# Optimization experiments

Hardware: AMD Instinct MI355X
Metric: run time of the kernel (lower is better)

Reference implementation:

```python
import jax, jax.numpy as jnp
import numpy as np

HEAD_NUM = 16
EMB_DIM = 1024
PROJ_DIM = 1024
CONTEXT_LEN = 2048
HEAD_DIM = PROJ_DIM // HEAD_NUM


def setup_inputs() -> dict:
    key = jax.random.key(0)
    k_x, k_q, k_k, k_v, k_o = jax.random.split(key, 5)
    scale = 0.02
    X_emb = jax.random.normal(k_x, (2, CONTEXT_LEN, EMB_DIM), dtype=jnp.float32)
    W_q = jax.random.normal(k_q, (EMB_DIM, PROJ_DIM), dtype=jnp.float32) * scale
    W_k = jax.random.normal(k_k, (EMB_DIM, PROJ_DIM), dtype=jnp.float32) * scale
    W_v = jax.random.normal(k_v, (EMB_DIM, PROJ_DIM), dtype=jnp.float32) * scale
    W_out = jax.random.normal(k_o, (PROJ_DIM, PROJ_DIM), dtype=jnp.float32) * scale
    return {"X_emb": X_emb, "W_q": W_q, "W_k": W_k, "W_v": W_v, "W_out": W_out}


def reference(X_emb, W_q, W_k, W_v, W_out):
    B, S, _ = X_emb.shape
    H, D = HEAD_NUM, HEAD_DIM
    # QKV projections (no bias), split into heads: [B, H, S, D]
    q = (X_emb @ W_q).reshape(B, S, H, D).transpose(0, 2, 1, 3)
    k = (X_emb @ W_k).reshape(B, S, H, D).transpose(0, 2, 1, 3)
    v = (X_emb @ W_v).reshape(B, S, H, D).transpose(0, 2, 1, 3)
    # Raw scores [B, H, S, S]; causal mask applied BEFORE scaling (as in source;
    # -inf is invariant under the subsequent division so math matches).
    scores = jnp.einsum("bhqd,bhkd->bhqk", q, k)
    causal = jnp.triu(jnp.ones((S, S), dtype=bool), k=1)  # True above diagonal
    scores = jnp.where(causal, -jnp.inf, scores)
    scores = scores / jnp.asarray(np.sqrt(D), dtype=scores.dtype)
    att_w = jax.nn.softmax(scores, axis=-1)
    # dropout_rate = 0.0 -> identity
    ctx = jnp.einsum("bhqk,bhkd->bhqd", att_w, v)
    ctx = ctx.transpose(0, 2, 1, 3).reshape(B, S, H * D)
    return ctx @ W_out
```

## Files before the change

### kernel.cpp

```cpp
#include <hip/hip_runtime.h>
#include <stdint.h>

#define SEQ   2048
#define EMB   1024
#define PROJ  1024
#define HEADS 16
#define HD    64
#define BATCH 2
#define MROWS (BATCH * SEQ)
#define QKVN  3072

typedef __attribute__((ext_vector_type(8))) __bf16 bf16x8;
typedef __attribute__((ext_vector_type(4))) __bf16 bf16x4;
typedef __attribute__((ext_vector_type(4))) float  f32x4;

static __device__ __forceinline__ __bf16 f2b(float f) {
  union { float f; uint32_t u; } a; a.f = f;
  uint32_t r = a.u + 0x7FFFu + ((a.u >> 16) & 1u);
  union { uint16_t u; __bf16 b; } o; o.u = (uint16_t)(r >> 16);
  return o.b;
}

#define GLOAD_LDS16(gsrc, ldst)                                                \
  __builtin_amdgcn_global_load_lds(                                            \
      (const __attribute__((address_space(1))) void*)(gsrc),                   \
      (__attribute__((address_space(3))) void*)(ldst), 16, 0, 0)

__global__ void cast_f32_bf16(const float* __restrict__ in,
                              __bf16* __restrict__ out, int n) {
  int i = (blockIdx.x * blockDim.x + threadIdx.x) * 4;
  if (i + 3 < n) {
    float4 v = *reinterpret_cast<const float4*>(in + i);
    bf16x4 o;
    o[0] = f2b(v.x); o[1] = f2b(v.y); o[2] = f2b(v.z); o[3] = f2b(v.w);
    *reinterpret_cast<bf16x4*>(out + i) = o;
  }
}

__global__ void transpose_cast(const float* __restrict__ W0, const float* __restrict__ W1,
                               const float* __restrict__ W2, const float* __restrict__ W3,
                               __bf16* __restrict__ Tqkv, __bf16* __restrict__ To) {
  const float* W; __bf16* T;
  switch (blockIdx.z) {
    case 0: W = W0; T = Tqkv;                       break;
    case 1: W = W1; T = Tqkv + (size_t)1024 * 1024; break;
    case 2: W = W2; T = Tqkv + (size_t)2048 * 1024; break;
    default: W = W3; T = To;                        break;
  }
  __shared__ float tile[32][33];
  int k0 = blockIdx.x * 32, n0 = blockIdx.y * 32;
  int tx = threadIdx.x & 31, ty = threadIdx.x >> 5;
#pragma unroll
  for (int r = ty; r < 32; r += 8)
    tile[r][tx] = W[(size_t)(k0 + r) * 1024 + n0 + tx];
  __syncthreads();
#pragma unroll
  for (int r = ty; r < 32; r += 8)
    T[(size_t)(n0 + r) * 1024 + k0 + tx] = f2b(tile[tx][r]);
}

template <int BM, bool OUT_BF16, bool SCALE_Q, bool VSPLIT>
__global__ __launch_bounds__(256) void gemm_bt(const __bf16* __restrict__ A,
                                               const __bf16* __restrict__ Bt,
                                               void* __restrict__ Cout,
                                               __bf16* __restrict__ vt,
                                               int M, int N, int K) {
  constexpr int MI = BM / 32;
  __shared__ __align__(16) __bf16 As[BM * 32];
  __shared__ __align__(16) __bf16 Bs[128 * 32];
  const int t = threadIdx.x;
  const int lane = t & 63, w = t >> 6;
  const int g = lane >> 4, l15 = lane & 15;
  const int m0 = blockIdx.x * BM, n0 = blockIdx.y * 128;
  const int wr = w >> 1, wc = w & 1;

  f32x4 acc[MI][4];
#pragma unroll
  for (int i = 0; i < MI; i++)
#pragma unroll
    for (int j = 0; j < 4; j++) acc[i][j] = {0.f, 0.f, 0.f, 0.f};

  for (int k0 = 0; k0 < K; k0 += 32) {
    __syncthreads();
#pragma unroll
    for (int c = t; c < BM * 4; c += 256)
      GLOAD_LDS16(A + (size_t)(m0 + (c >> 2)) * K + k0 + (c & 3) * 8, As + c * 8);
#pragma unroll
    for (int c = t; c < 512; c += 256)
      GLOAD_LDS16(Bt + (size_t)(n0 + (c >> 2)) * K + k0 + (c & 3) * 8, Bs + c * 8);
    __syncthreads();

    bf16x8 af[MI], bfr[4];
#pragma unroll
    for (int mi = 0; mi < MI; mi++)
      af[mi] = *reinterpret_cast<const bf16x8*>(As + (wr * (BM / 2) + mi * 16 + l15) * 32 + g * 8);
#pragma unroll
    for (int ni = 0; ni < 4; ni++)
      bfr[ni] = *reinterpret_cast<const bf16x8*>(Bs + (wc * 64 + ni * 16 + l15) * 32 + g * 8);
#pragma unroll
    for (int mi = 0; mi < MI; mi++)
#pragma unroll
      for (int ni = 0; ni < 4; ni++)
        acc[mi][ni] = __builtin_amdgcn_mfma_f32_16x16x32_bf16(af[mi], bfr[ni], acc[mi][ni], 0, 0, 0);
  }

#pragma unroll
  for (int mi = 0; mi < MI; mi++)
#pragma unroll
    for (int ni = 0; ni < 4; ni++) {
      int row = m0 + wr * (BM / 2) + mi * 16 + g * 4;
      int col = n0 + wc * 64 + ni * 16 + l15;
      if (VSPLIT && col >= 2048) {
        int hd = col - 2048;
        int bb = row >> 11, ss = row & 2047;
        bf16x4 v4;
#pragma unroll
        for (int r = 0; r < 4; r++) v4[r] = f2b(acc[mi][ni][r]);
        *reinterpret_cast<bf16x4*>(vt + ((size_t)((bb * 16 + (hd >> 6)) * 64 + (hd & 63))) * 2048 + ss) = v4;
      } else {
#pragma unroll
        for (int r = 0; r < 4; r++) {
          float v = acc[mi][ni][r];
          if (SCALE_Q && col < 1024) v *= 0.125f;
          if (OUT_BF16)
            ((__bf16*)Cout)[(size_t)(row + r) * N + col] = f2b(v);
          else
            ((float*)Cout)[(size_t)(row + r) * N + col] = v;
        }
      }
    }
}

__global__ __launch_bounds__(256, 2) void attn_fwd(const __bf16* __restrict__ QKV,
                                                   const __bf16* __restrict__ Vt,
                                                   __bf16* __restrict__ ctx) {
  const int id = blockIdx.x;
  const int bh = (id & 7) * 4 + ((id >> 3) & 3);
  const int mi = 31 - (id >> 5);
  const int b = bh >> 4, h = bh & 15;
  const int tid = threadIdx.x, lane = tid & 63, w = tid >> 6;
  const int g = lane >> 4, l15 = lane & 15;

  __shared__ __align__(16) __bf16 Ks[2][64 * 64];
  __shared__ __align__(16) __bf16 Vs[2][64 * 64];
  __shared__ __align__(16) __bf16 P_lds[4][16][72];

  const __bf16* Qg  = QKV + (size_t)b * SEQ * QKVN + h * 64;
  const __bf16* Kg  = Qg + 1024;
  const __bf16* VtH = Vt + (size_t)bh * 64 * 2048;
  __bf16* Cg = ctx + (size_t)b * SEQ * 1024 + h * 64;

  const int r0 = tid >> 3, j0 = tid & 7;
  const int r1 = r0 + 32;
  const int ls0 = r0 * 64 + ((j0 ^ (r0 & 7)) * 8);
  const int ls1 = r1 * 64 + ((j0 ^ (r1 & 7)) * 8);
  const size_t gk0 = (size_t)r0 * QKVN + j0 * 8;
  const size_t gk1 = (size_t)r1 * QKVN + j0 * 8;
  const size_t gv0 = (size_t)r0 * 2048 + j0 * 8;
  const size_t gv1 = (size_t)r1 * 2048 + j0 * 8;
  const int xw = l15 & 7;

  const int qw = mi * 64 + 16 * w;
  const int Tm = mi + 1;

  bf16x8 qf[2];
#pragma unroll
  for (int ks = 0; ks < 2; ks++)
    qf[ks] = *reinterpret_cast<const bf16x8*>(
        Qg + (size_t)(qw + l15) * QKVN + ks * 32 + g * 8);

  f32x4 acco[4];
  float mrun = -1e30f, lrun = 0.f;
#pragma unroll
  for (int nd = 0; nd < 4; nd++) acco[nd] = {0.f, 0.f, 0.f, 0.f};

  {
    bf16x8 ka = *reinterpret_cast<const bf16x8*>(Kg + gk0);
    bf16x8 kb = *reinterpret_cast<const bf16x8*>(Kg + gk1);
    bf16x8 va = *reinterpret_cast<const bf16x8*>(VtH + gv0);
    bf16x8 vc = *reinterpret_cast<const bf16x8*>(VtH + gv1);
    *reinterpret_cast<bf16x8*>(Ks[0] + ls0) = ka;
    *reinterpret_cast<bf16x8*>(Ks[0] + ls1) = kb;
    *reinterpret_cast<bf16x8*>(Vs[0] + ls0) = va;
    *reinterpret_cast<bf16x8*>(Vs[0] + ls1) = vc;
  }
  __syncthreads();

  for (int it = 0; it < Tm; ++it) {
    const int cur = it & 1, nxt = cur ^ 1;
    const bool hn = (it + 1 < Tm);
    bf16x8 ka, kb, va, vc;
    if (hn) {
      const size_t kvn = (size_t)(it + 1) * 64;
      ka = *reinterpret_cast<const bf16x8*>(Kg + kvn * QKVN + gk0);
      kb = *reinterpret_cast<const bf16x8*>(Kg + kvn * QKVN + gk1);
      va = *reinterpret_cast<const bf16x8*>(VtH + kvn + gv0);
      vc = *reinterpret_cast<const bf16x8*>(VtH + kvn + gv1);
    }

    {
      const int kv0 = it * 64;
      const bool diag = (it == Tm - 1);
      const __bf16* Kc = Ks[cur];
      const __bf16* Vc = Vs[cur];

      bf16x8 kf[4][2], vb[4][2];
#pragma unroll
      for (int nb = 0; nb < 4; nb++) {
        const int row = (nb * 16 + l15) * 64;
#pragma unroll
        for (int ks = 0; ks < 2; ks++) {
          const int co = ((ks * 4 + g) ^ xw) * 8;
          kf[nb][ks] = *reinterpret_cast<const bf16x8*>(Kc + row + co);
          vb[nb][ks] = *reinterpret_cast<const bf16x8*>(Vc + row + co);
        }
      }

      f32x4 accS[4];
#pragma unroll
      for (int nb = 0; nb < 4; nb++) accS[nb] = {0.f, 0.f, 0.f, 0.f};
      __builtin_amdgcn_s_setprio(1);
#pragma unroll
      for (int nb = 0; nb < 4; nb++) {
        accS[nb] = __builtin_amdgcn_mfma_f32_16x16x32_bf16(kf[nb][0], qf[0], accS[nb], 0, 0, 0);
        accS[nb] = __builtin_amdgcn_mfma_f32_16x16x32_bf16(kf[nb][1], qf[1], accS[nb], 0, 0, 0);
      }
      __builtin_amdgcn_s_setprio(0);

      if (diag) {
        const int qi = qw + l15;
#pragma unroll
        for (int nb = 0; nb < 4; nb++)
#pragma unroll
          for (int r = 0; r < 4; r++) {
            int kvi = kv0 + nb * 16 + g * 4 + r;
            if (kvi > qi) accS[nb][r] = -1e30f;
          }
      }

      {
        float pmax = -1e30f;
#pragma unroll
        for (int nb = 0; nb < 4; nb++)
#pragma unroll
          for (int r = 0; r < 4; r++) pmax = fmaxf(pmax, accS[nb][r]);
        pmax = fmaxf(pmax, __shfl_xor(pmax, 16));
        pmax = fmaxf(pmax, __shfl_xor(pmax, 32));
        if (!__all(pmax <= mrun + 8.0f)) {
          float mnew = fmaxf(mrun, pmax);
          float corr = __expf(mrun - mnew);
          mrun = mnew;
          lrun *= corr;
#pragma unroll
          for (int r = 0; r < 4; r++) {
            float cr = __shfl(corr, (g << 4) + (g << 2) + r);
#pragma unroll
            for (int nd = 0; nd < 4; nd++) acco[nd][r] *= cr;
          }
        }
        float lsum = 0.f;
#pragma unroll
        for (int nb = 0; nb < 4; nb++) {
          bf16x4 pk;
#pragma unroll
          for (int r = 0; r < 4; r++) {
            float pv = __expf(accS[nb][r] - mrun);
            lsum += pv;
            pk[r] = (__bf16)pv;
          }
          *reinterpret_cast<bf16x4*>(&P_lds[w][l15][nb * 16 + g * 4]) = pk;
        }
        lsum += __shfl_xor(lsum, 16);
        lsum += __shfl_xor(lsum, 32);
        lrun += lsum;
      }

      {
        bf16x8 pa0 = *reinterpret_cast<const bf16x8*>(&P_lds[w][l15][g * 8]);
        bf16x8 pa1 = *reinterpret_cast<const bf16x8*>(&P_lds[w][l15][32 + g * 8]);
        __builtin_amdgcn_s_setprio(1);
#pragma unroll
        for (int nd = 0; nd < 4; nd++) {
          acco[nd] = __builtin_amdgcn_mfma_f32_16x16x32_bf16(pa0, vb[nd][0], acco[nd], 0, 0, 0);
          acco[nd] = __builtin_amdgcn_mfma_f32_16x16x32_bf16(pa1, vb[nd][1], acco[nd], 0, 0, 0);
        }
        __builtin_amdgcn_s_setprio(0);
      }
    }

    if (hn) {
      *reinterpret_cast<bf16x8*>(Ks[nxt] + ls0) = ka;
      *reinterpret_cast<bf16x8*>(Ks[nxt] + ls1) = kb;
      *reinterpret_cast<bf16x8*>(Vs[nxt] + ls0) = va;
      *reinterpret_cast<bf16x8*>(Vs[nxt] + ls1) = vc;
    }
    __syncthreads();
  }

  {
    float inv = 1.0f / lrun;
#pragma unroll
    for (int r = 0; r < 4; r++) {
      float ir = __shfl(inv, (g << 4) + (g << 2) + r);
      int qrow = qw + g * 4 + r;
#pragma unroll
      for (int nd = 0; nd < 4; nd++)
        Cg[(size_t)qrow * 1024 + nd * 16 + l15] = (__bf16)(acco[nd][r] * ir);
    }
  }
}

extern "C" void kernel_launch(void* const* d_in, const int* in_sizes, int n_in,
                              void* d_out, int out_size, void* d_ws, size_t ws_size,
                              hipStream_t stream) {
  const float* X  = (const float*)d_in[0];
  const float* Wq = (const float*)d_in[1];
  const float* Wk = (const float*)d_in[2];
  const float* Wv = (const float*)d_in[3];
  const float* Wo = (const float*)d_in[4];
  float* out = (float*)d_out;

  uint8_t* ws = (uint8_t*)d_ws;
  size_t off = 0;
  const size_t actBytes = (size_t)MROWS * 1024 * 2;
  __bf16* Xb    = (__bf16*)(ws + off); off += actBytes;
  __bf16* WqkvT = (__bf16*)(ws + off); off += (size_t)QKVN * 1024 * 2;
  __bf16* WoT   = (__bf16*)(ws + off); off += (size_t)1024 * 1024 * 2;
  __bf16* QKV   = (__bf16*)(ws + off); off += (size_t)MROWS * QKVN * 2;
  __bf16* Vt    = (__bf16*)(ws + off); off += actBytes;
  __bf16* Cb    = Xb;

  cast_f32_bf16<<<dim3(MROWS * 1024 / 4 / 256), dim3(256), 0, stream>>>(X, Xb, MROWS * 1024);
  transpose_cast<<<dim3(32, 32, 4), dim3(256), 0, stream>>>(Wq, Wk, Wv, Wo, WqkvT, WoT);

  gemm_bt<128, true, true, true><<<dim3(MROWS / 128, QKVN / 128), dim3(256), 0, stream>>>(
      Xb, WqkvT, QKV, Vt, MROWS, QKVN, EMB);

  attn_fwd<<<dim3(1024), dim3(256), 0, stream>>>(QKV, Vt, Cb);

  gemm_bt<64, false, false, false><<<dim3(MROWS / 64, PROJ / 128), dim3(256), 0, stream>>>(
      Cb, WoT, out, nullptr, MROWS, PROJ, PROJ);
}
```

Measured before the change: 108.4 us.

## Pair complementary causal query tiles per attention block to balance and share KV loads

New measurement: 112.5 us. +3.8%, slower.

```diff
diff --git a/kernel.cpp b/kernel.cpp
--- a/kernel.cpp
+++ b/kernel.cpp
@@ -135,15 +135,23 @@
                                                    const __bf16* __restrict__ Vt,
                                                    __bf16* __restrict__ ctx) {
   const int id = blockIdx.x;
-  const int bh = (id & 7) * 4 + ((id >> 3) & 3);
-  const int mi = 31 - (id >> 5);
+  const int wx = id >> 3;
+  const int k5 = wx & 31;
+  const int bh = (id & 7) * 4 + (k5 & 3);
+  const int q8 = k5 >> 2;
+  const int pp = (wx >> 5) ? (15 - q8) : q8;
   const int b = bh >> 4, h = bh & 15;
   const int tid = threadIdx.x, lane = tid & 63, w = tid >> 6;
   const int g = lane >> 4, l15 = lane & 15;
 
+  const int ma = pp;
+  const int mb = 31 - pp;
+  const int Ta = pp + 1;
+  const int Tb = 32 - pp;
+
   __shared__ __align__(16) __bf16 Ks[2][64 * 64];
   __shared__ __align__(16) __bf16 Vs[2][64 * 64];
-  __shared__ __align__(16) __bf16 P_lds[4][16][72];
+  __shared__ __align__(16) __bf16 P_lds[4][2][16][72];
 
   const __bf16* Qg  = QKV + (size_t)b * SEQ * QKVN + h * 64;
   const __bf16* Kg  = Qg + 1024;
@@ -160,19 +168,25 @@
   const size_t gv1 = (size_t)r1 * 2048 + j0 * 8;
   const int xw = l15 & 7;
 
-  const int qw = mi * 64 + 16 * w;
-  const int Tm = mi + 1;
-
-  bf16x8 qf[2];
-#pragma unroll
-  for (int ks = 0; ks < 2; ks++)
-    qf[ks] = *reinterpret_cast<const bf16x8*>(
-        Qg + (size_t)(qw + l15) * QKVN + ks * 32 + g * 8);
-
-  f32x4 acco[4];
-  float mrun = -1e30f, lrun = 0.f;
-#pragma unroll
-  for (int nd = 0; nd < 4; nd++) acco[nd] = {0.f, 0.f, 0.f, 0.f};
+  const int qwb = mb * 64 + 16 * w;
+  const int qwa = ma * 64 + 16 * w;
+
+  bf16x8 qf[2][2];
+#pragma unroll
+  for (int ks = 0; ks < 2; ks++) {
+    qf[0][ks] = *reinterpret_cast<const bf16x8*>(
+        Qg + (size_t)(qwb + l15) * QKVN + ks * 32 + g * 8);
+    qf[1][ks] = *reinterpret_cast<const bf16x8*>(
+        Qg + (size_t)(qwa + l15) * QKVN + ks * 32 + g * 8);
+  }
+
+  f32x4 acco[2][4];
+  float mrun[2] = {-1e30f, -1e30f};
+  float lrun[2] = {0.f, 0.f};
+#pragma unroll
+  for (int m = 0; m < 2; m++)
+#pragma unroll
+    for (int nd = 0; nd < 4; nd++) acco[m][nd] = {0.f, 0.f, 0.f, 0.f};
 
   {
     bf16x8 ka = *reinterpret_cast<const bf16x8*>(Kg + gk0);
@@ -186,9 +200,9 @@
   }
   __syncthreads();
 
-  for (int it = 0; it < Tm; ++it) {
+  for (int it = 0; it < Tb; ++it) {
     const int cur = it & 1, nxt = cur ^ 1;
-    const bool hn = (it + 1 < Tm);
+    const bool hn = (it + 1 < Tb);
     bf16x8 ka, kb, va, vc;
     if (hn) {
       const size_t kvn = (size_t)(it + 1) * 64;
@@ -200,62 +214,80 @@
 
     {
       const int kv0 = it * 64;
-      const bool diag = (it == Tm - 1);
+      const bool act1 = (it < Ta);
       const __bf16* Kc = Ks[cur];
       const __bf16* Vc = Vs[cur];
 
-      bf16x8 kf[4][2], vb[4][2];
+      bf16x8 kf[4][2];
 #pragma unroll
       for (int nb = 0; nb < 4; nb++) {
         const int row = (nb * 16 + l15) * 64;
 #pragma unroll
-        for (int ks = 0; ks < 2; ks++) {
-          const int co = ((ks * 4 + g) ^ xw) * 8;
-          kf[nb][ks] = *reinterpret_cast<const bf16x8*>(Kc + row + co);
-          vb[nb][ks] = *reinterpret_cast<const bf16x8*>(Vc + row + co);
-        }
-      }
-
-      f32x4 accS[4];
-#pragma unroll
-      for (int nb = 0; nb < 4; nb++) accS[nb] = {0.f, 0.f, 0.f, 0.f};
+        for (int ks = 0; ks < 2; ks++)
+          kf[nb][ks] = *reinterpret_cast<const bf16x8*>(Kc + row + (((ks * 4 + g) ^ xw) * 8));
+      }
+
+      f32x4 accS[2][4];
+#pragma unroll
+      for (int m = 0; m < 2; m++)
+#pragma unroll
+        for (int nb = 0; nb < 4; nb++) accS[m][nb] = {0.f, 0.f, 0.f, 0.f};
       __builtin_amdgcn_s_setprio(1);
 #pragma unroll
       for (int nb = 0; nb < 4; nb++) {
-        accS[nb] = __builtin_amdgcn_mfma_f32_16x16x32_bf16(kf[nb][0], qf[0], accS[nb], 0, 0, 0);
-        accS[nb] = __builtin_amdgcn_mfma_f32_16x16x32_bf16(kf[nb][1], qf[1], accS[nb], 0, 0, 0);
+        accS[0][nb] = __builtin_amdgcn_mfma_f32_16x16x32_bf16(kf[nb][0], qf[0][0], accS[0][nb], 0, 0, 0);
+        accS[0][nb] = __builtin_amdgcn_mfma_f32_16x16x32_bf16(kf[nb][1], qf[0][1], accS[0][nb], 0, 0, 0);
+      }
+      if (act1) {
+#pragma unroll
+        for (int nb = 0; nb < 4; nb++) {
+          accS[1][nb] = __builtin_amdgcn_mfma_f32_16x16x32_bf16(kf[nb][0], qf[1][0], accS[1][nb], 0, 0, 0);
+          accS[1][nb] = __builtin_amdgcn_mfma_f32_16x16x32_bf16(kf[nb][1], qf[1][1], accS[1][nb], 0, 0, 0);
+        }
       }
       __builtin_amdgcn_s_setprio(0);
 
-      if (diag) {
-        const int qi = qw + l15;
+      if (it == Tb - 1) {
+        const int qi = qwb + l15;
 #pragma unroll
         for (int nb = 0; nb < 4; nb++)
 #pragma unroll
           for (int r = 0; r < 4; r++) {
             int kvi = kv0 + nb * 16 + g * 4 + r;
-            if (kvi > qi) accS[nb][r] = -1e30f;
-          }
-      }
-
-      {
+            if (kvi > qi) accS[0][nb][r] = -1e30f;
+          }
+      }
+      if (it == Ta - 1) {
+        const int qi = qwa + l15;
+#pragma unroll
+        for (int nb = 0; nb < 4; nb++)
+#pragma unroll
+          for (int r = 0; r < 4; r++) {
+            int kvi = kv0 + nb * 16 + g * 4 + r;
+            if (kvi > qi) accS[1][nb][r] = -1e30f;
+          }
+      }
+
+#pragma unroll
+      for (int m = 0; m < 2; m++) {
+        if (m == 1 && !act1) break;
         float pmax = -1e30f;
 #pragma unroll
         for (int nb = 0; nb < 4; nb++)
 #pragma unroll
-          for (int r = 0; r < 4; r++) pmax = fmaxf(pmax, accS[nb][r]);
+          for (int r = 0; r < 4; r++) pmax = fmaxf(pmax, accS[m][nb][r]);
         pmax = fmaxf(pmax, __shfl_xor(pmax, 16));
         pmax = fmaxf(pmax, __shfl_xor(pmax, 32));
-        if (!__all(pmax <= mrun + 8.0f)) {
-          float mnew = fmaxf(mrun, pmax);
-          float corr = __expf(mrun - mnew);
-          mrun = mnew;
-          lrun *= corr;
+        if (!__all(pmax <= mrun[m] + 8.0f)) {
+          float mnew = fmaxf(mrun[m], pmax);
+          float corr = __expf(mrun[m] - mnew);
+          mrun[m] = mnew;
+          lrun[m] *= corr;
 #pragma unroll
           for (int r = 0; r < 4; r++) {
             float cr = __shfl(corr, (g << 4) + (g << 2) + r);
 #pragma unroll
-            for (int nd = 0; nd < 4; nd++) acco[nd][r] *= cr;
+            for (int nd = 0; nd < 4; nd++) acco[m][nd][r] *= cr;
           }
         }
         float lsum = 0.f;
@@ -264,27 +296,46 @@
           bf16x4 pk;
 #pragma unroll
           for (int r = 0; r < 4; r++) {
-            float pv = __expf(accS[nb][r] - mrun);
+            float pv = __expf(accS[m][nb][r] - mrun[m]);
             lsum += pv;
             pk[r] = (__bf16)pv;
           }
-          *reinterpret_cast<bf16x4*>(&P_lds[w][l15][nb * 16 + g * 4]) = pk;
+          *reinterpret_cast<bf16x4*>(&P_lds[w][m][l15][nb * 16 + g * 4]) = pk;
         }
         lsum += __shfl_xor(lsum, 16);
         lsum += __shfl_xor(lsum, 32);
-        lrun += lsum;
+        lrun[m] += lsum;
       }
 
       {
-        bf16x8 pa0 = *reinterpret_cast<const bf16x8*>(&P_lds[w][l15][g * 8]);
-        bf16x8 pa1 = *reinterpret_cast<const bf16x8*>(&P_lds[w][l15][32 + g * 8]);
+        bf16x8 vb[4][2];
+#pragma unroll
+        for (int nb = 0; nb < 4; nb++) {
+          const int row = (nb * 16 + l15) * 64;
+#pragma unroll
+          for (int ks = 0; ks < 2; ks++)
+            vb[nb][ks] = *reinterpret_cast<const bf16x8*>(Vc + row + (((ks * 4 + g) ^ xw) * 8));
+        }
+        bf16x8 pa0 = *reinterpret_cast<const bf16x8*>(&P_lds[w][0][l15][g * 8]);
+        bf16x8 pa1 = *reinterpret_cast<const bf16x8*>(&P_lds[w][0][l15][32 + g * 8]);
         __builtin_amdgcn_s_setprio(1);
 #pragma unroll
         for (int nd = 0; nd < 4; nd++) {
-          acco[nd] = __builtin_amdgcn_mfma_f32_16x16x32_bf16(pa0, vb[nd][0], acco[nd], 0, 0, 0);
-          acco[nd] = __builtin_amdgcn_mfma_f32_16x16x32_bf16(pa1, vb[nd][1], acco[nd], 0, 0, 0);
+          acco[0][nd] = __builtin_amdgcn_mfma_f32_16x16x32_bf16(pa0, vb[nd][0], acco[0][nd], 0, 0, 0);
+          acco[0][nd] = __builtin_amdgcn_mfma_f32_16x16x32_bf16(pa1, vb[nd][1], acco[0][nd], 0, 0, 0);
         }
         __builtin_amdgcn_s_setprio(0);
+        if (act1) {
+          bf16x8 pb0 = *reinterpret_cast<const bf16x8*>(&P_lds[w][1][l15][g * 8]);
+          bf16x8 pb1 = *reinterpret_cast<const bf16x8*>(&P_lds[w][1][l15][32 + g * 8]);
+          __builtin_amdgcn_s_setprio(1);
+#pragma unroll
+          for (int nd = 0; nd < 4; nd++) {
+            acco[1][nd] = __builtin_amdgcn_mfma_f32_16x16x32_bf16(pb0, vb[nd][0], acco[1][nd], 0, 0, 0);
+            acco[1][nd] = __builtin_amdgcn_mfma_f32_16x16x32_bf16(pb1, vb[nd][1], acco[1][nd], 0, 0, 0);
+          }
+          __builtin_amdgcn_s_setprio(0);
+        }
       }
     }
 
@@ -297,15 +348,17 @@
     __syncthreads();
   }
 
-  {
-    float inv = 1.0f / lrun;
+#pragma unroll
+  for (int m = 0; m < 2; m++) {
+    const int qw = m ? qwa : qwb;
+    float inv = 1.0f / lrun[m];
 #pragma unroll
     for (int r = 0; r < 4; r++) {
       float ir = __shfl(inv, (g << 4) + (g << 2) + r);
       int qrow = qw + g * 4 + r;
 #pragma unroll
       for (int nd = 0; nd < 4; nd++)
-        Cg[(size_t)qrow * 1024 + nd * 16 + l15] = (__bf16)(acco[nd][r] * ir);
+        Cg[(size_t)qrow * 1024 + nd * 16 + l15] = (__bf16)(acco[m][nd][r] * ir);
     }
   }
 }
@@ -336,7 +389,7 @@
   gemm_bt<128, true, true, true><<<dim3(MROWS / 128, QKVN / 128), dim3(256), 0, stream>>>(
       Xb, WqkvT, QKV, Vt, MROWS, QKVN, EMB);
 
-  attn_fwd<<<dim3(1024), dim3(256), 0, stream>>>(QKV, Vt, Cb);
+  attn_fwd<<<dim3(512), dim3(256), 0, stream>>>(QKV, Vt, Cb);
 
   gemm_bt<64, false, false, false><<<dim3(MROWS / 64, PROJ / 128), dim3(256), 0, stream>>>(
       Cb, WoT, out, nullptr, MROWS, PROJ, PROJ);
```
